# Kernel tuning notes

Hardware: AMD Instinct MI355X
Metric: run time of the kernel (lower is better)

Reference implementation:

```python
import jax, jax.numpy as jnp
import numpy as np

DT = 0.5
NE, NIN = 400, 784
# excitatory LIF
THRESH_E, OFFSET, VRESET_E, EREST_E, REFRAC_E, TAU_MEM_E = -52.0, 20.0, -65.0, -65.0, 5.0, 100.0
# inhibitory LIF
THRESH_I, VRESET_I, EREST_I, REFRAC_I, TAU_MEM_I = -40.0, -45.0, -60.0, 2.0, 10.0
# synapses
TAU_SYN_E, TAU_SYN_I = 1.0, 2.0
E_EI, E_IE, E_EE = 0.0, -100.0, 0.0
# STDP
TC_P1, TC_P2, TC_PRE = 20.0, 40.0, 20.0
NU_PRE, NU_POST, WMAX = 0.0001, 0.01, 1.0
THETA0 = 20.0


def lif_step(mem, rc, I, thresh, v_reset, erest, tau, refrac):
    # conductance-based LIF with refractory period (inferred LIFei semantics)
    active = rc <= 0.0
    mem = jnp.where(active, mem + (erest - mem + I) * (DT / tau), mem)
    rc = jnp.maximum(rc - DT, 0.0)
    spike = (active & (mem > thresh)).astype(mem.dtype)
    fired = spike > 0.0
    mem = jnp.where(fired, v_reset, mem)
    rc = jnp.where(fired, refrac, rc)
    return mem, rc, spike


def setup_inputs() -> dict:
    key = jax.random.key(0)
    k1, k2 = jax.random.split(key)
    x = jax.random.uniform(k1, (50, 512, NIN), dtype=jnp.float32)  # Poisson-rate encoded frames
    W_ine = (jax.random.uniform(k2, (NE, NIN), dtype=jnp.float32) + 0.01) * 0.3  # create_ine
    W_ei = jnp.eye(NE, dtype=jnp.float32) * 10.4                                  # create_ei
    W_ie = (jnp.ones((NE, NE), jnp.float32) - jnp.eye(NE, dtype=jnp.float32)) * 17.0  # create_ie
    return {"x": x, "W_ine": W_ine, "W_ei": W_ei, "W_ie": W_ie}


def reference(x, W_ine, W_ei, W_ie):
    T, B, _ = x.shape
    z_e = jnp.zeros((B, NE), x.dtype)

    def step(carry, xt_t):
        xt, t = xt_t
        (W, g_ine, g_ei, g_ie, Iie, mem_e, rc_e, mem_i, rc_i,
         theta, tr_pre, tp1, tp2) = carry
        # normweight: rows sum to 78.4
        W = W / (jnp.sum(W, axis=1, keepdims=True) / 78.4)
        # input -> e synapse (STDP-plastic)
        dg_ine = xt @ W.T                         # (B, NE)
        I_ine = g_ine * (E_EE - mem_e)            # g=0 at t=0 -> I=0 (matches None init)
        g_ine = g_ine + (dg_ine - g_ine) * (DT / TAU_SYN_E)
        # excitatory LIF with adaptive threshold
        thr_e = THRESH_E - OFFSET + theta
        mem_e, rc_e, spike_e = lif_step(mem_e, rc_e, I_ine + Iie, thr_e,
                                        VRESET_E, EREST_E, TAU_MEM_E, REFRAC_E)
        # e -> i synapse
        dg_ei = spike_e @ W_ei.T
        I_ei = g_ei * (E_EI - mem_i)
        g_ei = g_ei + (dg_ei - g_ei) * (DT / TAU_SYN_E)
        # inhibitory LIF
        mem_i, rc_i, spike_i = lif_step(mem_i, rc_i, I_ei, THRESH_I,
                                        VRESET_I, EREST_I, TAU_MEM_I, REFRAC_I)
        # i -> e synapse (current fed into NEXT step's lif_e)
        dg_ie = spike_i @ W_ie.T
        Iie = g_ie * (E_IE - mem_e)
        g_ie = g_ie + (dg_ie - g_ie) * (DT / TAU_SYN_I)
        # threshold homeostasis
        theta = theta * (1.0 - DT / 1e7) + 0.05 * spike_e
        # pre trace: first call copies x, later decay then set to 1 where x>0.9
        tr_pre_upd = jnp.where(xt > 0.9, 1.0, tr_pre * (1.0 - DT / TC_PRE))
        tr_pre = jnp.where(t == 0, xt, tr_pre_upd)
        # post traces: return decayed value, then set to 1 where spike
        ret1 = tp1 * (1.0 - DT / TC_P1)
        ret2 = tp2 * (1.0 - DT / TC_P2)
        fired = spike_e > 0.9
        tp1 = jnp.where(fired, 1.0, ret1)
        tp2 = jnp.where(fired, 1.0, ret2)
        # STDP: autograd.grad of dg=x@W^T w.r.t. W with grad_outputs G is G^T @ x
        dw = (NU_PRE * jnp.einsum('be,bi->ei', ret1, xt)
              + NU_POST * jnp.einsum('be,bi->ei', spike_e * ret2, tr_pre))
        W = jnp.clip(W + dw, 0.0, WMAX)
        new_carry = (W, g_ine, g_ei, g_ie, Iie, mem_e, rc_e, mem_i, rc_i,
                     theta, tr_pre, tp1, tp2)
        return new_carry, spike_e

    carry0 = (W_ine,
              z_e, z_e, z_e,                      # g_ine, g_ei, g_ie
              z_e,                                # Iie
              jnp.full((B, NE), EREST_E, x.dtype), z_e,   # mem_e, rc_e
              jnp.full((B, NE), EREST_I, x.dtype), z_e,   # mem_i, rc_i
              jnp.full((B, NE), THETA0, x.dtype),         # theta
              jnp.zeros((B, NIN), x.dtype),               # trace_pre
              z_e, z_e)                                   # trace_post1/2
    _, spikes = jax.lax.scan(step, carry0, (x, jnp.arange(T)))
    return spikes  # (T, B, NE)
```

## Files before the change

### kernel.cpp

```cpp
#include <hip/hip_runtime.h>

#define NE 400
#define NIN 784
#define BB 512
#define TT 50

#define KC1 7
#define KCH1 112
#define KC2 4
#define KCH2 128

constexpr float C_KE     = (float)(0.5 / 100.0);
constexpr float C_KI     = (float)(0.5 / 10.0);
constexpr float C_GSE    = 0.5f;
constexpr float C_GSI    = 0.25f;
constexpr float C_DECTH  = (float)(1.0 - 0.5 / 1e7);
constexpr float C_DEC1   = (float)(1.0 - 0.5 / 20.0);
constexpr float C_DEC2   = (float)(1.0 - 0.5 / 40.0);
constexpr float C_DECPRE = (float)(1.0 - 0.5 / 20.0);
constexpr float C_NUPRE  = (float)0.0001;
constexpr float C_NUPOST = 0.01f;

__global__ void k_init(float* g_ine, float* g_ei, float* g_ie, float* Iie,
                       float* mem_e, float* rc_e, float* mem_i, float* rc_i,
                       float* theta, float* tp1, float* tp2) {
    int i = blockIdx.x * blockDim.x + threadIdx.x;
    if (i < BB * NE) {
        g_ine[i] = 0.f; g_ei[i] = 0.f; g_ie[i] = 0.f; Iie[i] = 0.f;
        mem_e[i] = -65.0f; rc_e[i] = 0.f;
        mem_i[i] = -60.0f; rc_i[i] = 0.f;
        theta[i] = 20.0f; tp1[i] = 0.f; tp2[i] = 0.f;
    }
}

__global__ __launch_bounds__(256) void k_rowsum0(const float* __restrict__ W,
                                                 float* __restrict__ d) {
    int e = blockIdx.x, tid = threadIdx.x;
    __shared__ float red[256];
    float s = 0.f;
    if (tid < 196) {
        float4 w = *(const float4*)&W[e * NIN + tid * 4];
        s = w.x + w.y + w.z + w.w;
    }
    red[tid] = s;
    __syncthreads();
    for (int off = 128; off > 0; off >>= 1) {
        if (tid < off) red[tid] += red[tid + off];
        __syncthreads();
    }
    if (tid == 0) d[e] = red[0] / 78.4f;
}

__global__ __launch_bounds__(256) void k_gemm1(const float* __restrict__ x,
                                               const float* __restrict__ W,
                                               float* __restrict__ dgp) {
    __shared__ float xs[16][68];
    __shared__ float ws[16][68];
    int tx = threadIdx.x & 15, ty = threadIdx.x >> 4;
    int lid = threadIdx.x;
    int e0 = blockIdx.x * 64, b0 = blockIdx.y * 64;
    int kbase = blockIdx.z * KCH1;

    float acc[4][4];
#pragma unroll
    for (int r = 0; r < 4; r++)
#pragma unroll
        for (int c = 0; c < 4; c++) acc[r][c] = 0.f;

    for (int kt = 0; kt < KCH1; kt += 16) {
        int k0 = kbase + kt;
        {
            int r = lid >> 2, cb = (lid & 3) * 4;
            float4 xv = *(const float4*)&x[(b0 + r) * NIN + k0 + cb];
            xs[cb + 0][r] = xv.x; xs[cb + 1][r] = xv.y;
            xs[cb + 2][r] = xv.z; xs[cb + 3][r] = xv.w;
            float4 wv;
            if (e0 + r < NE) wv = *(const float4*)&W[(e0 + r) * NIN + k0 + cb];
            else wv = make_float4(0.f, 0.f, 0.f, 0.f);
            ws[cb + 0][r] = wv.x; ws[cb + 1][r] = wv.y;
            ws[cb + 2][r] = wv.z; ws[cb + 3][r] = wv.w;
        }
        __syncthreads();
#pragma unroll
        for (int k = 0; k < 16; k++) {
            float4 av = *(const float4*)&xs[k][ty * 4];
            float4 bv = *(const float4*)&ws[k][tx * 4];
            float a[4] = {av.x, av.y, av.z, av.w};
            float b[4] = {bv.x, bv.y, bv.z, bv.w};
#pragma unroll
            for (int r = 0; r < 4; r++)
#pragma unroll
                for (int c = 0; c < 4; c++) acc[r][c] += a[r] * b[c];
        }
        __syncthreads();
    }
    if (e0 + tx * 4 < NE) {
        float* base = dgp + (size_t)blockIdx.z * BB * NE;
#pragma unroll
        for (int r = 0; r < 4; r++) {
            float4 v = make_float4(acc[r][0], acc[r][1], acc[r][2], acc[r][3]);
            *(float4*)&base[(b0 + ty * 4 + r) * NE + e0 + tx * 4] = v;
        }
    }
}

__global__ __launch_bounds__(512) void k_mid(const float* __restrict__ dgp,
                                             const float* __restrict__ d,
                                             const float* __restrict__ xt,
                                             float* __restrict__ tr, int t,
                                             float* g_ine, float* g_ei, float* g_ie,
                                             float* Iie, float* mem_e, float* rc_e,
                                             float* mem_i, float* rc_i, float* theta,
                                             float* tp1, float* tp2,
                                             float* __restrict__ A1,
                                             float* __restrict__ A2,
                                             float* __restrict__ out_t) {
    if (blockIdx.x >= BB) {
        int base = (blockIdx.x - BB) * 2048 + threadIdx.x * 4;
        float4 xv = *(const float4*)&xt[base];
        float4 o;
        if (t == 0) {
            o = xv;
        } else {
            float4 tv = *(const float4*)&tr[base];
            o.x = (xv.x > 0.9f) ? 1.0f : tv.x * C_DECPRE;
            o.y = (xv.y > 0.9f) ? 1.0f : tv.y * C_DECPRE;
            o.z = (xv.z > 0.9f) ? 1.0f : tv.z * C_DECPRE;
            o.w = (xv.w > 0.9f) ? 1.0f : tv.w * C_DECPRE;
        }
        *(float4*)&tr[base] = o;
        return;
    }
    int b = blockIdx.x;
    int e = threadIdx.x;
    __shared__ float red[512];
    int idx = b * NE + e;

    float spk_i = 0.f, spk_e = 0.f;
    float g1 = 0.f, me = 0.f, re = 0.f, th = 0.f, g2 = 0.f, mi = 0.f, ri = 0.f;

    if (e < NE) {
        float dg = 0.f;
#pragma unroll
        for (int c = 0; c < KC1; c++) dg += dgp[(size_t)c * BB * NE + idx];
        dg = dg / d[e];
        g1 = g_ine[idx]; me = mem_e[idx]; re = rc_e[idx];
        th = theta[idx];
        float Ii = Iie[idx];
        float I_in = g1 * (0.0f - me);
        g1 = g1 + (dg - g1) * C_GSE;
        bool act = (re <= 0.0f);
        float I = I_in + Ii;
        if (act) me = me + ((-65.0f - me) + I) * C_KE;
        re = fmaxf(re - 0.5f, 0.0f);
        float thr = -72.0f + th;
        spk_e = (act && (me > thr)) ? 1.0f : 0.0f;
        if (spk_e > 0.0f) { me = -65.0f; re = 5.0f; }
        float dgei = spk_e * 10.4f;
        g2 = g_ei[idx]; mi = mem_i[idx]; ri = rc_i[idx];
        float I_ei = g2 * (0.0f - mi);
        g2 = g2 + (dgei - g2) * C_GSE;
        bool ai = (ri <= 0.0f);
        if (ai) mi = mi + ((-60.0f - mi) + I_ei) * C_KI;
        ri = fmaxf(ri - 0.5f, 0.0f);
        spk_i = (ai && (mi > -40.0f)) ? 1.0f : 0.0f;
        if (spk_i > 0.0f) { mi = -45.0f; ri = 2.0f; }
    }
    red[e] = spk_i;
    __syncthreads();
    for (int off = 256; off > 0; off >>= 1) {
        if (e < off) red[e] += red[e + off];
        __syncthreads();
    }
    float S = red[0];
    if (e < NE) {
        float dgie = 17.0f * (S - spk_i);
        float g3 = g_ie[idx];
        float Iie_new = g3 * (-100.0f - me);
        g3 = g3 + (dgie - g3) * C_GSI;
        th = th * C_DECTH + 0.05f * spk_e;
        float r1 = tp1[idx] * C_DEC1;
        float r2 = tp2[idx] * C_DEC2;
        bool fired = spk_e > 0.9f;
        A1[idx] = r1;
        A2[idx] = spk_e * r2;
        tp1[idx] = fired ? 1.0f : r1;
        tp2[idx] = fired ? 1.0f : r2;
        g_ine[idx] = g1; g_ei[idx] = g2; g_ie[idx] = g3; Iie[idx] = Iie_new;
        mem_e[idx] = me; rc_e[idx] = re; mem_i[idx] = mi; rc_i[idx] = ri;
        theta[idx] = th;
        out_t[idx] = spk_e;
    }
}

__global__ __launch_bounds__(256) void k_gemm2(const float* __restrict__ A1,
                                               const float* __restrict__ A2,
                                               const float* __restrict__ xt,
                                               const float* __restrict__ tr,
                                               float* __restrict__ part) {
    __shared__ float a1s[16][68];
    __shared__ float a2s[16][68];
    __shared__ float xs[16][68];
    __shared__ float ts[16][68];
    int tx = threadIdx.x & 15, ty = threadIdx.x >> 4;
    int lid = threadIdx.x;
    int i0 = blockIdx.x * 64, e0 = blockIdx.y * 64;
    int bbase = blockIdx.z * KCH2;

    float s1[4][4], s2[4][4];
#pragma unroll
    for (int r = 0; r < 4; r++)
#pragma unroll
        for (int c = 0; c < 4; c++) { s1[r][c] = 0.f; s2[r][c] = 0.f; }

    for (int bt = 0; bt < KCH2; bt += 16) {
        int b0 = bbase + bt;
        {
            int r = lid >> 4, cb = (lid & 15) * 4;
            float4 v1, v2;
            if (e0 + cb < NE) {
                v1 = *(const float4*)&A1[(b0 + r) * NE + e0 + cb];
                v2 = *(const float4*)&A2[(b0 + r) * NE + e0 + cb];
            } else {
                v1 = make_float4(0.f, 0.f, 0.f, 0.f);
                v2 = v1;
            }
            *(float4*)&a1s[r][cb] = v1;
            *(float4*)&a2s[r][cb] = v2;
            float4 xv, tv;
            if (i0 + cb < NIN) {
                xv = *(const float4*)&xt[(b0 + r) * NIN + i0 + cb];
                tv = *(const float4*)&tr[(b0 + r) * NIN + i0 + cb];
            } else {
                xv = make_float4(0.f, 0.f, 0.f, 0.f);
                tv = xv;
            }
            *(float4*)&xs[r][cb] = xv;
            *(float4*)&ts[r][cb] = tv;
        }
        __syncthreads();
#pragma unroll
        for (int k = 0; k < 16; k++) {
            float4 a1v = *(const float4*)&a1s[k][ty * 4];
            float4 a2v = *(const float4*)&a2s[k][ty * 4];
            float4 xv = *(const float4*)&xs[k][tx * 4];
            float4 tv = *(const float4*)&ts[k][tx * 4];
            float a1[4] = {a1v.x, a1v.y, a1v.z, a1v.w};
            float a2[4] = {a2v.x, a2v.y, a2v.z, a2v.w};
            float xx[4] = {xv.x, xv.y, xv.z, xv.w};
            float tt[4] = {tv.x, tv.y, tv.z, tv.w};
#pragma unroll
            for (int r = 0; r < 4; r++)
#pragma unroll
                for (int c = 0; c < 4; c++) {
                    s1[r][c] += a1[r] * xx[c];
                    s2[r][c] += a2[r] * tt[c];
                }
        }
        __syncthreads();
    }
    if (e0 + ty * 4 < NE && i0 + tx * 4 < NIN) {
        float* base = part + (size_t)blockIdx.z * NE * NIN;
#pragma unroll
        for (int r = 0; r < 4; r++) {
            float4 v = make_float4(C_NUPRE * s1[r][0] + C_NUPOST * s2[r][0],
                                   C_NUPRE * s1[r][1] + C_NUPOST * s2[r][1],
                                   C_NUPRE * s1[r][2] + C_NUPOST * s2[r][2],
                                   C_NUPRE * s1[r][3] + C_NUPOST * s2[r][3]);
            *(float4*)&base[(e0 + ty * 4 + r) * NIN + i0 + tx * 4] = v;
        }
    }
}

__global__ __launch_bounds__(256) void k_wupdate(float* __restrict__ W,
                                                 const float* __restrict__ part,
                                                 float* __restrict__ d) {
    int e = blockIdx.x, tid = threadIdx.x;
    __shared__ float red[256];
    float dv = d[e];
    float s = 0.f;
    if (tid < 196) {
        int off = e * NIN + tid * 4;
        float4 w = *(const float4*)&W[off];
        float4 acc = make_float4(w.x / dv, w.y / dv, w.z / dv, w.w / dv);
#pragma unroll
        for (int c = 0; c < KC2; c++) {
            float4 p = *(const float4*)&part[(size_t)c * NE * NIN + off];
            acc.x += p.x; acc.y += p.y; acc.z += p.z; acc.w += p.w;
        }
        acc.x = fminf(fmaxf(acc.x, 0.f), 1.f);
        acc.y = fminf(fmaxf(acc.y, 0.f), 1.f);
        acc.z = fminf(fmaxf(acc.z, 0.f), 1.f);
        acc.w = fminf(fmaxf(acc.w, 0.f), 1.f);
        *(float4*)&W[off] = acc;
        s = acc.x + acc.y + acc.z + acc.w;
    }
    red[tid] = s;
    __syncthreads();
    for (int off = 128; off > 0; off >>= 1) {
        if (tid < off) red[tid] += red[tid + off];
        __syncthreads();
    }
    if (tid == 0) d[e] = red[0] / 78.4f;
}

extern "C" void kernel_launch(void* const* d_in, const int* in_sizes, int n_in,
                              void* d_out, int out_size, void* d_ws, size_t ws_size,
                              hipStream_t stream) {
    const float* x     = (const float*)d_in[0];
    const float* W_ine = (const float*)d_in[1];

    float* p = (float*)d_ws;
    float* W_cur = p; p += NE * NIN;
    float* dbuf  = p; p += NE;
    float* dgp   = p; p += (size_t)KC1 * BB * NE;
    float* part  = p; p += (size_t)KC2 * NE * NIN;
    float* A1    = p; p += BB * NE;
    float* A2    = p; p += BB * NE;
    float* g_ine = p; p += BB * NE;
    float* g_ei  = p; p += BB * NE;
    float* g_ie  = p; p += BB * NE;
    float* Iie   = p; p += BB * NE;
    float* mem_e = p; p += BB * NE;
    float* rc_e  = p; p += BB * NE;
    float* mem_i = p; p += BB * NE;
    float* rc_i  = p; p += BB * NE;
    float* theta = p; p += BB * NE;
    float* tp1   = p; p += BB * NE;
    float* tp2   = p; p += BB * NE;
    float* tr    = p; p += BB * NIN;

    hipMemcpyAsync(W_cur, W_ine, (size_t)NE * NIN * sizeof(float),
                   hipMemcpyDeviceToDevice, stream);
    k_init<<<(BB * NE + 255) / 256, 256, 0, stream>>>(g_ine, g_ei, g_ie, Iie, mem_e,
                                                      rc_e, mem_i, rc_i, theta, tp1, tp2);
    k_rowsum0<<<NE, 256, 0, stream>>>(W_cur, dbuf);

    for (int t = 0; t < TT; t++) {
        const float* xt = x + (size_t)t * BB * NIN;
        float* out_t = (float*)d_out + (size_t)t * BB * NE;
        k_gemm1<<<dim3(7, 8, KC1), 256, 0, stream>>>(xt, W_cur, dgp);
        k_mid<<<BB + 196, 512, 0, stream>>>(dgp, dbuf, xt, tr, t, g_ine, g_ei, g_ie,
                                            Iie, mem_e, rc_e, mem_i, rc_i, theta,
                                            tp1, tp2, A1, A2, out_t);
        k_gemm2<<<dim3(13, 7, KC2), 256, 0, stream>>>(A1, A2, xt, tr, part);
        k_wupdate<<<NE, 256, 0, stream>>>(W_cur, part, dbuf);
    }
}
```

Baseline: 2.607 ms.

## Fuse weight update and row-sum into first GEMM, prefetch tiles, drop extra launches

Folds the per-step weight update (normalize, add STDP partials, clip) and the row-sum computation into the loading stage of the first GEMM, writing updated weights to a ping-pong buffer and per-chunk row sums that the mid kernel reduces into the normalizer. This removes the separate wupdate and rowsum kernels, the initial memcpy, and the last unused gemm2 launch. Both GEMMs gain register prefetch of the next tile, and the mid kernel uses a wavefront shuffle reduction. In exchange, each gemm1 block recomputes the weight update for its tile across all batch-row blocks, adding redundant reads of the partial buffers.

```diff
diff --git a/kernel.cpp b/kernel.cpp
--- a/kernel.cpp
+++ b/kernel.cpp
@@ -33,54 +33,70 @@
     }
 }
 
-__global__ __launch_bounds__(256) void k_rowsum0(const float* __restrict__ W,
-                                                 float* __restrict__ d) {
-    int e = blockIdx.x, tid = threadIdx.x;
-    __shared__ float red[256];
-    float s = 0.f;
-    if (tid < 196) {
-        float4 w = *(const float4*)&W[e * NIN + tid * 4];
-        s = w.x + w.y + w.z + w.w;
-    }
-    red[tid] = s;
-    __syncthreads();
-    for (int off = 128; off > 0; off >>= 1) {
-        if (tid < off) red[tid] += red[tid + off];
-        __syncthreads();
-    }
-    if (tid == 0) d[e] = red[0] / 78.4f;
-}
-
-__global__ __launch_bounds__(256) void k_gemm1(const float* __restrict__ x,
-                                               const float* __restrict__ W,
-                                               float* __restrict__ dgp) {
+__global__ __launch_bounds__(256) void k_g1(const float* __restrict__ x,
+                                            const float* __restrict__ Wprev,
+                                            const float* __restrict__ part,
+                                            const float* __restrict__ dvec,
+                                            float* __restrict__ Wout,
+                                            float* __restrict__ rs,
+                                            float* __restrict__ dgp, int t) {
     __shared__ float xs[16][68];
     __shared__ float ws[16][68];
-    int tx = threadIdx.x & 15, ty = threadIdx.x >> 4;
+    __shared__ float rsh[4][64];
     int lid = threadIdx.x;
+    int tx = lid & 15, ty = lid >> 4;
     int e0 = blockIdx.x * 64, b0 = blockIdx.y * 64;
     int kbase = blockIdx.z * KCH1;
+    int r = lid >> 2, cb = (lid & 3) * 4;
+    int erow = e0 + r;
+    bool ev = erow < NE;
+    float dval = 1.0f;
+    if (t > 0 && ev) dval = dvec[erow];
 
     float acc[4][4];
 #pragma unroll
-    for (int r = 0; r < 4; r++)
-#pragma unroll
-        for (int c = 0; c < 4; c++) acc[r][c] = 0.f;
-
-    for (int kt = 0; kt < KCH1; kt += 16) {
-        int k0 = kbase + kt;
-        {
-            int r = lid >> 2, cb = (lid & 3) * 4;
-            float4 xv = *(const float4*)&x[(b0 + r) * NIN + k0 + cb];
-            xs[cb + 0][r] = xv.x; xs[cb + 1][r] = xv.y;
-            xs[cb + 2][r] = xv.z; xs[cb + 3][r] = xv.w;
-            float4 wv;
-            if (e0 + r < NE) wv = *(const float4*)&W[(e0 + r) * NIN + k0 + cb];
-            else wv = make_float4(0.f, 0.f, 0.f, 0.f);
-            ws[cb + 0][r] = wv.x; ws[cb + 1][r] = wv.y;
-            ws[cb + 2][r] = wv.z; ws[cb + 3][r] = wv.w;
-        }
-        __syncthreads();
+    for (int a = 0; a < 4; a++)
+#pragma unroll
+        for (int b = 0; b < 4; b++) acc[a][b] = 0.f;
+    float rsacc = 0.f;
+
+    float4 xv, wn;
+    auto loadt = [&](int kt) {
+        int k0 = kbase + kt * 16;
+        xv = *(const float4*)&x[(b0 + r) * NIN + k0 + cb];
+        if (ev) {
+            float4 w = *(const float4*)&Wprev[erow * NIN + k0 + cb];
+            if (t > 0) {
+                int o = erow * NIN + k0 + cb;
+                float4 s = make_float4(w.x / dval, w.y / dval, w.z / dval, w.w / dval);
+#pragma unroll
+                for (int c = 0; c < KC2; c++) {
+                    float4 p = *(const float4*)&part[c * NE * NIN + o];
+                    s.x += p.x; s.y += p.y; s.z += p.z; s.w += p.w;
+                }
+                w.x = fminf(fmaxf(s.x, 0.f), 1.f);
+                w.y = fminf(fmaxf(s.y, 0.f), 1.f);
+                w.z = fminf(fmaxf(s.z, 0.f), 1.f);
+                w.w = fminf(fmaxf(s.w, 0.f), 1.f);
+            }
+            wn = w;
+        } else {
+            wn = make_float4(0.f, 0.f, 0.f, 0.f);
+        }
+    };
+
+    loadt(0);
+    for (int kt = 0; kt < KCH1 / 16; kt++) {
+        xs[cb + 0][r] = xv.x; xs[cb + 1][r] = xv.y;
+        xs[cb + 2][r] = xv.z; xs[cb + 3][r] = xv.w;
+        ws[cb + 0][r] = wn.x; ws[cb + 1][r] = wn.y;
+        ws[cb + 2][r] = wn.z; ws[cb + 3][r] = wn.w;
+        if (blockIdx.y == 0 && ev) {
+            *(float4*)&Wout[erow * NIN + kbase + kt * 16 + cb] = wn;
+            rsacc += (wn.x + wn.y) + (wn.z + wn.w);
+        }
+        __syncthreads();
+        if (kt < KCH1 / 16 - 1) loadt(kt + 1);
 #pragma unroll
         for (int k = 0; k < 16; k++) {
             float4 av = *(const float4*)&xs[k][ty * 4];
@@ -88,26 +104,36 @@
             float a[4] = {av.x, av.y, av.z, av.w};
             float b[4] = {bv.x, bv.y, bv.z, bv.w};
 #pragma unroll
-            for (int r = 0; r < 4; r++)
-#pragma unroll
-                for (int c = 0; c < 4; c++) acc[r][c] += a[r] * b[c];
-        }
-        __syncthreads();
-    }
+            for (int p = 0; p < 4; p++)
+#pragma unroll
+                for (int q = 0; q < 4; q++) acc[p][q] += a[p] * b[q];
+        }
+        __syncthreads();
+    }
+
+    if (blockIdx.y == 0) {
+        rsh[lid & 3][r] = rsacc;
+        __syncthreads();
+        if (lid < 64 && e0 + lid < NE)
+            rs[blockIdx.z * NE + e0 + lid] =
+                (rsh[0][lid] + rsh[1][lid]) + (rsh[2][lid] + rsh[3][lid]);
+    }
+
     if (e0 + tx * 4 < NE) {
-        float* base = dgp + (size_t)blockIdx.z * BB * NE;
-#pragma unroll
-        for (int r = 0; r < 4; r++) {
-            float4 v = make_float4(acc[r][0], acc[r][1], acc[r][2], acc[r][3]);
-            *(float4*)&base[(b0 + ty * 4 + r) * NE + e0 + tx * 4] = v;
+        float* base = dgp + blockIdx.z * BB * NE;
+#pragma unroll
+        for (int p = 0; p < 4; p++) {
+            float4 v = make_float4(acc[p][0], acc[p][1], acc[p][2], acc[p][3]);
+            *(float4*)&base[(b0 + ty * 4 + p) * NE + e0 + tx * 4] = v;
         }
     }
 }
 
 __global__ __launch_bounds__(512) void k_mid(const float* __restrict__ dgp,
-                                             const float* __restrict__ d,
+                                             const float* __restrict__ rs,
                                              const float* __restrict__ xt,
                                              float* __restrict__ tr, int t,
+                                             float* __restrict__ dvec,
                                              float* g_ine, float* g_ei, float* g_ie,
                                              float* Iie, float* mem_e, float* rc_e,
                                              float* mem_i, float* rc_i, float* theta,
@@ -133,17 +159,22 @@
     }
     int b = blockIdx.x;
     int e = threadIdx.x;
-    __shared__ float red[512];
+    __shared__ float red[8];
     int idx = b * NE + e;
 
     float spk_i = 0.f, spk_e = 0.f;
     float g1 = 0.f, me = 0.f, re = 0.f, th = 0.f, g2 = 0.f, mi = 0.f, ri = 0.f;
 
     if (e < NE) {
+        float dsum = 0.f;
+#pragma unroll
+        for (int c = 0; c < KC1; c++) dsum += rs[c * NE + e];
+        float dv = dsum / 78.4f;
+        if (b == 0) dvec[e] = dv;
         float dg = 0.f;
 #pragma unroll
-        for (int c = 0; c < KC1; c++) dg += dgp[(size_t)c * BB * NE + idx];
-        dg = dg / d[e];
+        for (int c = 0; c < KC1; c++) dg += dgp[c * BB * NE + idx];
+        dg = dg / dv;
         g1 = g_ine[idx]; me = mem_e[idx]; re = rc_e[idx];
         th = theta[idx];
         float Ii = Iie[idx];
@@ -166,13 +197,13 @@
         spk_i = (ai && (mi > -40.0f)) ? 1.0f : 0.0f;
         if (spk_i > 0.0f) { mi = -45.0f; ri = 2.0f; }
     }
-    red[e] = spk_i;
+    float v = spk_i;
+#pragma unroll
+    for (int o = 32; o > 0; o >>= 1) v += __shfl_down(v, o, 64);
+    if ((e & 63) == 0) red[e >> 6] = v;
     __syncthreads();
-    for (int off = 256; off > 0; off >>= 1) {
-        if (e < off) red[e] += red[e + off];
-        __syncthreads();
-    }
-    float S = red[0];
+    float S = ((red[0] + red[1]) + (red[2] + red[3])) +
+              ((red[4] + red[5]) + (red[6] + red[7]));
     if (e < NE) {
         float dgie = 17.0f * (S - spk_i);
         float g3 = g_ie[idx];
@@ -206,102 +237,72 @@
     int lid = threadIdx.x;
     int i0 = blockIdx.x * 64, e0 = blockIdx.y * 64;
     int bbase = blockIdx.z * KCH2;
+    int r = lid >> 4, cb = (lid & 15) * 4;
 
     float s1[4][4], s2[4][4];
 #pragma unroll
-    for (int r = 0; r < 4; r++)
-#pragma unroll
-        for (int c = 0; c < 4; c++) { s1[r][c] = 0.f; s2[r][c] = 0.f; }
-
-    for (int bt = 0; bt < KCH2; bt += 16) {
-        int b0 = bbase + bt;
-        {
-            int r = lid >> 4, cb = (lid & 15) * 4;
-            float4 v1, v2;
-            if (e0 + cb < NE) {
-                v1 = *(const float4*)&A1[(b0 + r) * NE + e0 + cb];
-                v2 = *(const float4*)&A2[(b0 + r) * NE + e0 + cb];
-            } else {
-                v1 = make_float4(0.f, 0.f, 0.f, 0.f);
-                v2 = v1;
-            }
-            *(float4*)&a1s[r][cb] = v1;
-            *(float4*)&a2s[r][cb] = v2;
-            float4 xv, tv;
-            if (i0 + cb < NIN) {
-                xv = *(const float4*)&xt[(b0 + r) * NIN + i0 + cb];
-                tv = *(const float4*)&tr[(b0 + r) * NIN + i0 + cb];
-            } else {
-                xv = make_float4(0.f, 0.f, 0.f, 0.f);
-                tv = xv;
-            }
-            *(float4*)&xs[r][cb] = xv;
-            *(float4*)&ts[r][cb] = tv;
-        }
-        __syncthreads();
+    for (int a = 0; a < 4; a++)
+#pragma unroll
+        for (int b = 0; b < 4; b++) { s1[a][b] = 0.f; s2[a][b] = 0.f; }
+
+    float4 v1, v2, xv, tv;
+    auto loadt = [&](int bt) {
+        int b0 = bbase + bt * 16;
+        if (e0 + cb < NE) {
+            v1 = *(const float4*)&A1[(b0 + r) * NE + e0 + cb];
+            v2 = *(const float4*)&A2[(b0 + r) * NE + e0 + cb];
+        } else {
+            v1 = make_float4(0.f, 0.f, 0.f, 0.f);
+            v2 = v1;
+        }
+        if (i0 + cb < NIN) {
+            xv = *(const float4*)&xt[(b0 + r) * NIN + i0 + cb];
+            tv = *(const float4*)&tr[(b0 + r) * NIN + i0 + cb];
+        } else {
+            xv = make_float4(0.f, 0.f, 0.f, 0.f);
+            tv = xv;
+        }
+    };
+
+    loadt(0);
+    for (int bt = 0; bt < KCH2 / 16; bt++) {
+        *(float4*)&a1s[r][cb] = v1;
+        *(float4*)&a2s[r][cb] = v2;
+        *(float4*)&xs[r][cb] = xv;
+        *(float4*)&ts[r][cb] = tv;
+        __syncthreads();
+        if (bt < KCH2 / 16 - 1) loadt(bt + 1);
 #pragma unroll
         for (int k = 0; k < 16; k++) {
             float4 a1v = *(const float4*)&a1s[k][ty * 4];
             float4 a2v = *(const float4*)&a2s[k][ty * 4];
-            float4 xv = *(const float4*)&xs[k][tx * 4];
-            float4 tv = *(const float4*)&ts[k][tx * 4];
+            float4 xvv = *(const float4*)&xs[k][tx * 4];
+            float4 tvv = *(const float4*)&ts[k][tx * 4];
             float a1[4] = {a1v.x, a1v.y, a1v.z, a1v.w};
             float a2[4] = {a2v.x, a2v.y, a2v.z, a2v.w};
-            float xx[4] = {xv.x, xv.y, xv.z, xv.w};
-            float tt[4] = {tv.x, tv.y, tv.z, tv.w};
-#pragma unroll
-            for (int r = 0; r < 4; r++)
-#pragma unroll
-                for (int c = 0; c < 4; c++) {
-                    s1[r][c] += a1[r] * xx[c];
-                    s2[r][c] += a2[r] * tt[c];
+            float xx[4] = {xvv.x, xvv.y, xvv.z, xvv.w};
+            float tt[4] = {tvv.x, tvv.y, tvv.z, tvv.w};
+#pragma unroll
+            for (int p = 0; p < 4; p++)
+#pragma unroll
+                for (int q = 0; q < 4; q++) {
+                    s1[p][q] += a1[p] * xx[q];
+                    s2[p][q] += a2[p] * tt[q];
                 }
         }
         __syncthreads();
     }
     if (e0 + ty * 4 < NE && i0 + tx * 4 < NIN) {
-        float* base = part + (size_t)blockIdx.z * NE * NIN;
-#pragma unroll
-        for (int r = 0; r < 4; r++) {
-            float4 v = make_float4(C_NUPRE * s1[r][0] + C_NUPOST * s2[r][0],
-                                   C_NUPRE * s1[r][1] + C_NUPOST * s2[r][1],
-                                   C_NUPRE * s1[r][2] + C_NUPOST * s2[r][2],
-                                   C_NUPRE * s1[r][3] + C_NUPOST * s2[r][3]);
-            *(float4*)&base[(e0 + ty * 4 + r) * NIN + i0 + tx * 4] = v;
-        }
-    }
-}
-
-__global__ __launch_bounds__(256) void k_wupdate(float* __restrict__ W,
-                                                 const float* __restrict__ part,
-                                                 float* __restrict__ d) {
-    int e = blockIdx.x, tid = threadIdx.x;
-    __shared__ float red[256];
-    float dv = d[e];
-    float s = 0.f;
-    if (tid < 196) {
-        int off = e * NIN + tid * 4;
-        float4 w = *(const float4*)&W[off];
-        float4 acc = make_float4(w.x / dv, w.y / dv, w.z / dv, w.w / dv);
-#pragma unroll
-        for (int c = 0; c < KC2; c++) {
-            float4 p = *(const float4*)&part[(size_t)c * NE * NIN + off];
-            acc.x += p.x; acc.y += p.y; acc.z += p.z; acc.w += p.w;
-        }
-        acc.x = fminf(fmaxf(acc.x, 0.f), 1.f);
-        acc.y = fminf(fmaxf(acc.y, 0.f), 1.f);
-        acc.z = fminf(fmaxf(acc.z, 0.f), 1.f);
-        acc.w = fminf(fmaxf(acc.w, 0.f), 1.f);
-        *(float4*)&W[off] = acc;
-        s = acc.x + acc.y + acc.z + acc.w;
-    }
-    red[tid] = s;
-    __syncthreads();
-    for (int off = 128; off > 0; off >>= 1) {
-        if (tid < off) red[tid] += red[tid + off];
-        __syncthreads();
-    }
-    if (tid == 0) d[e] = red[0] / 78.4f;
+        float* base = part + blockIdx.z * NE * NIN;
+#pragma unroll
+        for (int p = 0; p < 4; p++) {
+            float4 v = make_float4(C_NUPRE * s1[p][0] + C_NUPOST * s2[p][0],
+                                   C_NUPRE * s1[p][1] + C_NUPOST * s2[p][1],
+                                   C_NUPRE * s1[p][2] + C_NUPOST * s2[p][2],
+                                   C_NUPRE * s1[p][3] + C_NUPOST * s2[p][3]);
+            *(float4*)&base[(e0 + ty * 4 + p) * NIN + i0 + tx * 4] = v;
+        }
+    }
 }
 
 extern "C" void kernel_launch(void* const* d_in, const int* in_sizes, int n_in,
@@ -311,10 +312,12 @@
     const float* W_ine = (const float*)d_in[1];
 
     float* p = (float*)d_ws;
-    float* W_cur = p; p += NE * NIN;
+    float* wbuf0 = p; p += NE * NIN;
+    float* wbuf1 = p; p += NE * NIN;
+    float* rs    = p; p += KC1 * NE;
     float* dbuf  = p; p += NE;
-    float* dgp   = p; p += (size_t)KC1 * BB * NE;
-    float* part  = p; p += (size_t)KC2 * NE * NIN;
+    float* dgp   = p; p += KC1 * BB * NE;
+    float* part  = p; p += KC2 * NE * NIN;
     float* A1    = p; p += BB * NE;
     float* A2    = p; p += BB * NE;
     float* g_ine = p; p += BB * NE;
@@ -330,20 +333,19 @@
     float* tp2   = p; p += BB * NE;
     float* tr    = p; p += BB * NIN;
 
-    hipMemcpyAsync(W_cur, W_ine, (size_t)NE * NIN * sizeof(float),
-                   hipMemcpyDeviceToDevice, stream);
     k_init<<<(BB * NE + 255) / 256, 256, 0, stream>>>(g_ine, g_ei, g_ie, Iie, mem_e,
                                                       rc_e, mem_i, rc_i, theta, tp1, tp2);
-    k_rowsum0<<<NE, 256, 0, stream>>>(W_cur, dbuf);
 
     for (int t = 0; t < TT; t++) {
         const float* xt = x + (size_t)t * BB * NIN;
         float* out_t = (float*)d_out + (size_t)t * BB * NE;
-        k_gemm1<<<dim3(7, 8, KC1), 256, 0, stream>>>(xt, W_cur, dgp);
-        k_mid<<<BB + 196, 512, 0, stream>>>(dgp, dbuf, xt, tr, t, g_ine, g_ei, g_ie,
+        const float* Wprev = (t == 0) ? W_ine : ((t & 1) ? wbuf0 : wbuf1);
+        float* Wout = (t & 1) ? wbuf1 : wbuf0;
+        k_g1<<<dim3(7, 8, KC1), 256, 0, stream>>>(xt, Wprev, part, dbuf, Wout, rs, dgp, t);
+        k_mid<<<BB + 196, 512, 0, stream>>>(dgp, rs, xt, tr, t, dbuf, g_ine, g_ei, g_ie,
                                             Iie, mem_e, rc_e, mem_i, rc_i, theta,
                                             tp1, tp2, A1, A2, out_t);
-        k_gemm2<<<dim3(13, 7, KC2), 256, 0, stream>>>(A1, A2, xt, tr, part);
-        k_wupdate<<<NE, 256, 0, stream>>>(W_cur, part, dbuf);
-    }
-}
+        if (t < TT - 1)
+            k_gemm2<<<dim3(13, 7, KC2), 256, 0, stream>>>(A1, A2, xt, tr, part);
+    }
+}
```

Result: slower. 2.888 ms (+10.8%).
